# Kernel optimization log

Measured on AMD Instinct MI355X. Metric: run time of the kernel, lower is better.

## Reference

```python
import jax, jax.numpy as jnp
import numpy as np

B, S, D, H = 4, 2048, 1024, 16
DH = D // H  # 64


def setup_inputs() -> dict:
    key = jax.random.key(0)
    ks = jax.random.split(key, 7)
    scale = 1.0 / np.sqrt(DH)  # ~ torch Linear init scale
    return {
        "seqs": jax.random.normal(ks[0], (B, S, D), dtype=jnp.float32),
        "Wq": jax.random.normal(ks[1], (H, DH, DH), dtype=jnp.float32) * scale,
        "bq": jax.random.normal(ks[2], (H, DH), dtype=jnp.float32) * scale,
        "Wk": jax.random.normal(ks[3], (H, DH, DH), dtype=jnp.float32) * scale,
        "bk": jax.random.normal(ks[4], (H, DH), dtype=jnp.float32) * scale,
        "Wv": jax.random.normal(ks[5], (H, DH, DH), dtype=jnp.float32) * scale,
        "bv": jax.random.normal(ks[6], (H, DH), dtype=jnp.float32) * scale,
    }


def reference(seqs, Wq, bq, Wk, bk, Wv, bv):
    # seqs: [B, S, D] -> per-head slices [B, S, H, DH]
    x = seqs.reshape(B, S, H, DH)
    # torch Linear: y = s @ W.T + b  (W: [out, in]) -> einsum over 'in' axis d
    q = jnp.einsum("bshd,hed->bshe", x, Wq) + bq  # [B,S,H,DH]
    k = jnp.einsum("bshd,hed->bshe", x, Wk) + bk
    v = jnp.einsum("bshd,hed->bshe", x, Wv) + bv
    inv_sqrt = 1.0 / jnp.sqrt(jnp.asarray(DH, dtype=seqs.dtype))
    scores = jnp.einsum("bshe,bthe->bhst", q, k) * inv_sqrt  # [B,H,S,S]
    attn = jax.nn.softmax(scores, axis=-1)
    out = jnp.einsum("bhst,bthe->bshe", attn, v)  # [B,S,H,DH]
    # torch.hstack over heads == concat along feature dim
    return out.reshape(B, S, D)
```

## Files before the change

kernel.cpp:

```cpp
#include <hip/hip_runtime.h>
#include <hip/hip_bf16.h>

#define NB 4
#define NS 2048
#define ND 1024
#define NH 16
#define NDH 64
#define SCF 0.18033688011112042f

typedef __attribute__((ext_vector_type(8))) short bf16x8;
typedef __attribute__((ext_vector_type(4))) float f32x4;

__device__ __forceinline__ float bf2f(unsigned short u) {
    union { unsigned int u; float f; } x; x.u = ((unsigned int)u) << 16; return x.f;
}
__device__ __forceinline__ unsigned short f2bf(float f) {
    union { float f; unsigned int u; } x; x.f = f;
    unsigned int r = x.u + 0x7FFFu + ((x.u >> 16) & 1u);
    return (unsigned short)(r >> 16);
}
__device__ __forceinline__ unsigned short f2bf_fast(float f) {
    union { float f; unsigned int u; } x; x.f = f;
    return (unsigned short)((x.u + 0x8000u) >> 16);
}
__device__ __forceinline__ unsigned int pkbf(float a, float b) {
    union { float f; unsigned int u; } x, y; x.f = a; y.f = b;
    return __builtin_amdgcn_perm(y.u + 0x8000u, x.u + 0x8000u, 0x07060302u);
}
__device__ __forceinline__ unsigned int pktr(float a, float b) {
    union { float f; unsigned int u; } x, y; x.f = a; y.f = b;
    return __builtin_amdgcn_perm(y.u, x.u, 0x07060302u);
}

__global__ __launch_bounds__(256) void convert_w_kernel(
    const unsigned short* __restrict__ x,
    const void* __restrict__ Wq, const void* __restrict__ bq,
    const void* __restrict__ Wk, const void* __restrict__ bk,
    const void* __restrict__ Wv, const void* __restrict__ bv,
    int* __restrict__ flag,
    unsigned short* __restrict__ Wb,
    unsigned short* __restrict__ Bb)
{
    __shared__ int sflag;
    const int tid = threadIdx.x;
    if (tid < 64) {
        int bad = 0, zer = 0;
        for (int i = tid; i < 1024; i += 64) {
            const unsigned short u = x[2 * i];
            const int e = (u >> 7) & 0xFF;
            if (e >= 0x8F) bad++;
            if (e == 0 && (u & 0x7F)) bad++;
            if (u == 0) zer++;
        }
        #pragma unroll
        for (int off = 1; off < 64; off <<= 1) {
            bad += __shfl_xor(bad, off, 64);
            zer += __shfl_xor(zer, off, 64);
        }
        if (tid == 0) {
            const int f = (bad > 64 || zer > 512) ? 1 : 0;
            sflag = f;
            flag[0] = f;
        }
    }
    __syncthreads();
    const int isf32 = sflag;

    const void* Wsrc[3] = { Wq, Wk, Wv };
    const void* Bsrc[3] = { bq, bk, bv };
    const int NW = 3 * 65536, NBIAS = 3 * 1024;
    for (int i = blockIdx.x * blockDim.x + tid; i < NW + NBIAS;
         i += gridDim.x * blockDim.x) {
        int m, off; const void* src; unsigned short* dst;
        if (i < NW) { m = i >> 16; off = i & 65535; src = Wsrc[m]; dst = Wb + i; }
        else { int j = i - NW; m = j >> 10; off = j & 1023; src = Bsrc[m];
               dst = Bb + j; }
        float v = isf32 ? ((const float*)src)[off]
                        : bf2f(((const unsigned short*)src)[off]);
        if (m == 0) v *= SCF;
        *dst = f2bf(v);
    }
}

__global__ __launch_bounds__(256) void qkv_proj_kernel(
    const unsigned short* __restrict__ x,
    const unsigned short* __restrict__ Wb,
    const unsigned short* __restrict__ Bb,
    const int* __restrict__ flag,
    unsigned short* __restrict__ Qw, unsigned short* __restrict__ Kw,
    unsigned short* __restrict__ VwT)
{
    __shared__ __align__(16) unsigned short Tl[3 * 64 * 72];

    const int isf32 = flag[0];
    const int tid  = threadIdx.x;
    const int wave = tid >> 6, lane = tid & 63;
    const int quad = lane >> 4, l16 = lane & 15;
    const int ttile = blockIdx.x, h = blockIdx.y;
    const int b  = ttile >> 5;
    const int s0 = (ttile & 31) * 64;
    const int bh = b * NH + h;

    const int tok_a = ttile * 64 + wave * 16 + l16;
    bf16x8 af0, af1;
    if (isf32) {
        const f32x4* xp = (const f32x4*)((const float*)x + (size_t)tok_a * ND + h * NDH);
        const f32x4 v0 = xp[quad * 2], v1 = xp[quad * 2 + 1];
        const f32x4 v2 = xp[8 + quad * 2], v3 = xp[8 + quad * 2 + 1];
        union { bf16x8 v; unsigned int d[4]; } a0, a1;
        a0.d[0] = pkbf(v0[0], v0[1]); a0.d[1] = pkbf(v0[2], v0[3]);
        a0.d[2] = pkbf(v1[0], v1[1]); a0.d[3] = pkbf(v1[2], v1[3]);
        a1.d[0] = pkbf(v2[0], v2[1]); a1.d[1] = pkbf(v2[2], v2[3]);
        a1.d[2] = pkbf(v3[0], v3[1]); a1.d[3] = pkbf(v3[2], v3[3]);
        af0 = a0.v; af1 = a1.v;
    } else {
        const unsigned short* xr = x + (size_t)tok_a * ND + h * NDH;
        af0 = *(const bf16x8*)(xr + quad * 8);
        af1 = *(const bf16x8*)(xr + 32 + quad * 8);
    }

    #pragma unroll
    for (int m = 0; m < 3; ++m) {
        const unsigned short* W = Wb + m * 65536 + h * 4096;
        unsigned short* R = Tl + m * (64 * 72);
        #pragma unroll
        for (int n = 0; n < 4; ++n) {
            const unsigned short* wrow = W + (n * 16 + l16) * NDH;
            const bf16x8 b0 = *(const bf16x8*)(wrow + quad * 8);
            const bf16x8 b1 = *(const bf16x8*)(wrow + 32 + quad * 8);
            f32x4 acc = {0.f, 0.f, 0.f, 0.f};
            acc = __builtin_amdgcn_mfma_f32_16x16x32_bf16(af0, b0, acc, 0, 0, 0);
            acc = __builtin_amdgcn_mfma_f32_16x16x32_bf16(af1, b1, acc, 0, 0, 0);
            const float bias = bf2f(Bb[m * 1024 + h * NDH + n * 16 + l16]);
            if (m < 2) {
                #pragma unroll
                for (int r = 0; r < 4; ++r) {
                    const int row = wave * 16 + quad * 4 + r;
                    R[row * 72 + n * 16 + l16] = f2bf_fast(acc[r] + bias);
                }
            } else {
                #pragma unroll
                for (int r = 0; r < 4; ++r) {
                    const int tok = wave * 16 + quad * 4 + r;
                    const int pc = ((tok & 15) << 2) | (tok >> 4);
                    R[(n * 16 + l16) * 72 + pc] = f2bf_fast(acc[r] + bias);
                }
            }
        }
    }
    __syncthreads();
    #pragma unroll
    for (int p = 0; p < 2; ++p) {
        const int ch = tid + p * 256;
        const int tl = ch >> 3, sub = ch & 7;
        *(bf16x8*)(Qw + ((size_t)bh * NS + s0 + tl) * NDH + sub * 8) =
            *(const bf16x8*)(Tl + tl * 72 + sub * 8);
        *(bf16x8*)(Kw + ((size_t)bh * NS + s0 + tl) * NDH + sub * 8) =
            *(const bf16x8*)(Tl + 64 * 72 + tl * 72 + sub * 8);
        *(bf16x8*)(VwT + ((size_t)bh * NDH + tl) * NS + s0 + sub * 8) =
            *(const bf16x8*)(Tl + 2 * 64 * 72 + tl * 72 + sub * 8);
    }
}

__global__ __launch_bounds__(256, 2) void attn_kernel(
    const unsigned short* __restrict__ Qw,
    const unsigned short* __restrict__ Kw,
    const unsigned short* __restrict__ VwT,
    const int* __restrict__ flag,
    unsigned short* __restrict__ out)
{
    __shared__ __align__(16) unsigned short smem[5 * 64 * 72];
    unsigned short* Pt = smem + 4 * 64 * 72;
    unsigned short* Ot = smem;

    const int isf32 = flag[0];
    const int tid  = threadIdx.x;
    const int wave = tid >> 6, lane = tid & 63;
    const int quad = lane >> 4, l16 = lane & 15;
    const int qt = blockIdx.x & 7;
    const int bh = blockIdx.x >> 3;
    const int b = bh >> 4, h = bh & 15;

    const unsigned short* Qb = Qw  + (size_t)bh * NS * NDH;
    const unsigned short* Kb = Kw  + (size_t)bh * NS * NDH;
    const unsigned short* Vb = VwT + (size_t)bh * NDH * NS;

    bf16x8 qf[4][2];
    #pragma unroll
    for (int mh = 0; mh < 4; ++mh) {
        const int tok = qt * 256 + wave * 64 + mh * 16 + l16;
        qf[mh][0] = *(const bf16x8*)(Qb + (size_t)tok * NDH + quad * 8);
        qf[mh][1] = *(const bf16x8*)(Qb + (size_t)tok * NDH + 32 + quad * 8);
    }

    f32x4 o[4][4];
    float os[4][4];
    #pragma unroll
    for (int mh = 0; mh < 4; ++mh) {
        #pragma unroll
        for (int n = 0; n < 4; ++n) o[mh][n] = f32x4{0.f, 0.f, 0.f, 0.f};
        #pragma unroll
        for (int r = 0; r < 4; ++r) os[mh][r] = 0.f;
    }

    const int stage_r = tid >> 3, stage_c = tid & 7;
    unsigned short* PtW = Pt + wave * (16 * 72);

    bf16x8 kpre[2], vpre[2];
    #pragma unroll
    for (int p = 0; p < 2; ++p) {
        const int rr = stage_r + p * 32;
        kpre[p] = *(const bf16x8*)(Kb + (size_t)rr * NDH + stage_c * 8);
        vpre[p] = *(const bf16x8*)(Vb + (size_t)rr * NS + stage_c * 8);
    }

    for (int kt = 0; kt < NS / 64; ++kt) {
        unsigned short* KB = smem + (kt & 1) * (64 * 72);
        unsigned short* VB = smem + (2 + (kt & 1)) * (64 * 72);
        #pragma unroll
        for (int p = 0; p < 2; ++p) {
            const int rr = stage_r + p * 32;
            *(bf16x8*)(KB + rr * 72 + stage_c * 8) = kpre[p];
            *(bf16x8*)(VB + rr * 72 + stage_c * 8) = vpre[p];
        }
        __syncthreads();
        if (kt + 1 < NS / 64) {
            #pragma unroll
            for (int p = 0; p < 2; ++p) {
                const int rr = stage_r + p * 32;
                kpre[p] = *(const bf16x8*)(Kb + (size_t)((kt + 1) * 64 + rr) * NDH + stage_c * 8);
                vpre[p] = *(const bf16x8*)(Vb + (size_t)rr * NS + (kt + 1) * 64 + stage_c * 8);
            }
        }

        bf16x8 kb[4][2], vb[4][2];
        #pragma unroll
        for (int n = 0; n < 4; ++n) {
            kb[n][0] = *(const bf16x8*)(KB + (n * 16 + l16) * 72 + quad * 8);
            kb[n][1] = *(const bf16x8*)(KB + (n * 16 + l16) * 72 + 32 + quad * 8);
            vb[n][0] = *(const bf16x8*)(VB + (n * 16 + l16) * 72 + quad * 8);
            vb[n][1] = *(const bf16x8*)(VB + (n * 16 + l16) * 72 + 32 + quad * 8);
        }

        #pragma unroll
        for (int mh = 0; mh < 4; ++mh) {
            f32x4 sf[4];
            #pragma unroll
            for (int n = 0; n < 4; ++n) {
                f32x4 acc = {0.f, 0.f, 0.f, 0.f};
                acc = __builtin_amdgcn_mfma_f32_16x16x32_bf16(qf[mh][0], kb[n][0], acc, 0, 0, 0);
                acc = __builtin_amdgcn_mfma_f32_16x16x32_bf16(qf[mh][1], kb[n][1], acc, 0, 0, 0);
                sf[n] = acc;
            }
            #pragma unroll
            for (int r = 0; r < 4; ++r) {
                const float p0 = __builtin_amdgcn_exp2f(sf[0][r]);
                const float p1 = __builtin_amdgcn_exp2f(sf[1][r]);
                const float p2 = __builtin_amdgcn_exp2f(sf[2][r]);
                const float p3 = __builtin_amdgcn_exp2f(sf[3][r]);
                os[mh][r] += (p0 + p1) + (p2 + p3);
                uint2 d; d.x = pktr(p0, p1); d.y = pktr(p2, p3);
                *(uint2*)(PtW + (quad * 4 + r) * 72 + l16 * 4) = d;
            }
            const bf16x8 pa0 = *(const bf16x8*)(PtW + l16 * 72 + quad * 8);
            const bf16x8 pa1 = *(const bf16x8*)(PtW + l16 * 72 + 32 + quad * 8);
            #pragma unroll
            for (int n = 0; n < 4; ++n) {
                o[mh][n] = __builtin_amdgcn_mfma_f32_16x16x32_bf16(pa0, vb[n][0], o[mh][n], 0, 0, 0);
                o[mh][n] = __builtin_amdgcn_mfma_f32_16x16x32_bf16(pa1, vb[n][1], o[mh][n], 0, 0, 0);
            }
        }
    }

    float inv[4][4];
    #pragma unroll
    for (int mh = 0; mh < 4; ++mh) {
        #pragma unroll
        for (int r = 0; r < 4; ++r) {
            float s = os[mh][r];
            #pragma unroll
            for (int off = 1; off < 16; off <<= 1)
                s += __shfl_xor(s, off, 64);
            inv[mh][r] = 1.0f / s;
        }
    }

    if (isf32) {
        float* of = (float*)out;
        #pragma unroll
        for (int mh = 0; mh < 4; ++mh) {
            #pragma unroll
            for (int r = 0; r < 4; ++r) {
                const int s = qt * 256 + wave * 64 + mh * 16 + quad * 4 + r;
                #pragma unroll
                for (int n = 0; n < 4; ++n)
                    of[((size_t)(b * NS + s)) * ND + h * NDH + n * 16 + l16] =
                        o[mh][n][r] * inv[mh][r];
            }
        }
    } else {
        __syncthreads();
        #pragma unroll
        for (int mh = 0; mh < 4; ++mh) {
            #pragma unroll
            for (int r = 0; r < 4; ++r) {
                const int row = wave * 64 + mh * 16 + quad * 4 + r;
                #pragma unroll
                for (int n = 0; n < 4; ++n)
                    Ot[row * 72 + n * 16 + l16] = f2bf(o[mh][n][r] * inv[mh][r]);
            }
        }
        __syncthreads();
        #pragma unroll
        for (int p = 0; p < 8; ++p) {
            const int ch = tid + p * 256;
            const int tl = ch >> 3, sub = ch & 7;
            const int s = qt * 256 + tl;
            *(bf16x8*)(out + ((size_t)(b * NS + s)) * ND + h * NDH + sub * 8) =
                *(const bf16x8*)(Ot + tl * 72 + sub * 8);
        }
    }
}

extern "C" void kernel_launch(void* const* d_in, const int* in_sizes, int n_in,
                              void* d_out, int out_size, void* d_ws, size_t ws_size,
                              hipStream_t stream)
{
    const unsigned short* x = (const unsigned short*)d_in[0];
    int* flag = (int*)d_ws;
    const size_t per = (size_t)NB * NH * NS * NDH;
    unsigned short* Qw  = (unsigned short*)((char*)d_ws + 256);
    unsigned short* Kw  = Qw + per;
    unsigned short* VwT = Kw + per;
    unsigned short* Wb  = VwT + per;
    unsigned short* Bb  = Wb + 3 * 65536;

    convert_w_kernel<<<256, 256, 0, stream>>>(
        x, d_in[1], d_in[2], d_in[3], d_in[4], d_in[5], d_in[6], flag, Wb, Bb);
    qkv_proj_kernel<<<dim3(NB * NS / 64, NH), 256, 0, stream>>>(
        x, Wb, Bb, flag, Qw, Kw, VwT);
    attn_kernel<<<NB * NH * (NS / 256), 256, 0, stream>>>(
        Qw, Kw, VwT, flag, (unsigned short*)d_out);
}
```

Before: 199.0 us.

## Load K/V fragments directly from global memory into registers, drop LDS staging

```diff
diff --git a/kernel.cpp b/kernel.cpp
--- a/kernel.cpp
+++ b/kernel.cpp
@@ -169,21 +169,22 @@
     const int* __restrict__ flag,
     unsigned short* __restrict__ out)
 {
-    __shared__ __align__(16) unsigned short smem[5 * 64 * 72];
-    unsigned short* Pt = smem + 4 * 64 * 72;
+    __shared__ __align__(16) unsigned short smem[256 * 72];
     unsigned short* Ot = smem;
 
     const int isf32 = flag[0];
     const int tid  = threadIdx.x;
     const int wave = tid >> 6, lane = tid & 63;
     const int quad = lane >> 4, l16 = lane & 15;
-    const int qt = blockIdx.x & 7;
-    const int bh = blockIdx.x >> 3;
+    const int bh = blockIdx.x & 63;
+    const int qt = blockIdx.x >> 6;
     const int b = bh >> 4, h = bh & 15;
 
     const unsigned short* Qb = Qw  + (size_t)bh * NS * NDH;
     const unsigned short* Kb = Kw  + (size_t)bh * NS * NDH;
     const unsigned short* Vb = VwT + (size_t)bh * NDH * NS;
+
+    unsigned short* PtW = smem + wave * (16 * 72);
 
     bf16x8 qf[4][2];
     #pragma unroll
@@ -203,53 +204,39 @@
         for (int r = 0; r < 4; ++r) os[mh][r] = 0.f;
     }
 
-    const int stage_r = tid >> 3, stage_c = tid & 7;
-    unsigned short* PtW = Pt + wave * (16 * 72);
-
-    bf16x8 kpre[2], vpre[2];
-    #pragma unroll
-    for (int p = 0; p < 2; ++p) {
-        const int rr = stage_r + p * 32;
-        kpre[p] = *(const bf16x8*)(Kb + (size_t)rr * NDH + stage_c * 8);
-        vpre[p] = *(const bf16x8*)(Vb + (size_t)rr * NS + stage_c * 8);
-    }
-
-    for (int kt = 0; kt < NS / 64; ++kt) {
-        unsigned short* KB = smem + (kt & 1) * (64 * 72);
-        unsigned short* VB = smem + (2 + (kt & 1)) * (64 * 72);
-        #pragma unroll
-        for (int p = 0; p < 2; ++p) {
-            const int rr = stage_r + p * 32;
-            *(bf16x8*)(KB + rr * 72 + stage_c * 8) = kpre[p];
-            *(bf16x8*)(VB + rr * 72 + stage_c * 8) = vpre[p];
-        }
-        __syncthreads();
-        if (kt + 1 < NS / 64) {
-            #pragma unroll
-            for (int p = 0; p < 2; ++p) {
-                const int rr = stage_r + p * 32;
-                kpre[p] = *(const bf16x8*)(Kb + (size_t)((kt + 1) * 64 + rr) * NDH + stage_c * 8);
-                vpre[p] = *(const bf16x8*)(Vb + (size_t)rr * NS + (kt + 1) * 64 + stage_c * 8);
-            }
-        }
-
-        bf16x8 kb[4][2], vb[4][2];
+    bf16x8 kA[4][2], kB[4][2], vb[4][2];
+
+    auto loadK = [&](bf16x8 (&kd)[4][2], const int t) {
+        const unsigned short* Kt =
+            Kb + (size_t)t * 64 * NDH + (size_t)l16 * NDH + quad * 8;
         #pragma unroll
         for (int n = 0; n < 4; ++n) {
-            kb[n][0] = *(const bf16x8*)(KB + (n * 16 + l16) * 72 + quad * 8);
-            kb[n][1] = *(const bf16x8*)(KB + (n * 16 + l16) * 72 + 32 + quad * 8);
-            vb[n][0] = *(const bf16x8*)(VB + (n * 16 + l16) * 72 + quad * 8);
-            vb[n][1] = *(const bf16x8*)(VB + (n * 16 + l16) * 72 + 32 + quad * 8);
-        }
-
+            kd[n][0] = *(const bf16x8*)(Kt + n * 16 * NDH);
+            kd[n][1] = *(const bf16x8*)(Kt + n * 16 * NDH + 32);
+        }
+    };
+    auto loadV = [&](const int t) {
+        const unsigned short* Vt =
+            Vb + (size_t)l16 * NS + (size_t)t * 64 + quad * 8;
+        #pragma unroll
+        for (int n = 0; n < 4; ++n) {
+            vb[n][0] = *(const bf16x8*)(Vt + (size_t)(n * 16) * NS);
+            vb[n][1] = *(const bf16x8*)(Vt + (size_t)(n * 16) * NS + 32);
+        }
+    };
+
+    auto body = [&](bf16x8 (&kc)[4][2], bf16x8 (&kn)[4][2], const int t) {
+        loadV(t);
+        const int tn = (t + 1 < NS / 64) ? t + 1 : NS / 64 - 1;
+        loadK(kn, tn);
         #pragma unroll
         for (int mh = 0; mh < 4; ++mh) {
             f32x4 sf[4];
             #pragma unroll
             for (int n = 0; n < 4; ++n) {
                 f32x4 acc = {0.f, 0.f, 0.f, 0.f};
-                acc = __builtin_amdgcn_mfma_f32_16x16x32_bf16(qf[mh][0], kb[n][0], acc, 0, 0, 0);
-                acc = __builtin_amdgcn_mfma_f32_16x16x32_bf16(qf[mh][1], kb[n][1], acc, 0, 0, 0);
+                acc = __builtin_amdgcn_mfma_f32_16x16x32_bf16(qf[mh][0], kc[n][0], acc, 0, 0, 0);
+                acc = __builtin_amdgcn_mfma_f32_16x16x32_bf16(qf[mh][1], kc[n][1], acc, 0, 0, 0);
                 sf[n] = acc;
             }
             #pragma unroll
@@ -270,6 +257,13 @@
                 o[mh][n] = __builtin_amdgcn_mfma_f32_16x16x32_bf16(pa1, vb[n][1], o[mh][n], 0, 0, 0);
             }
         }
+    };
+
+    loadK(kA, 0);
+    #pragma unroll 1
+    for (int t = 0; t < NS / 64; t += 2) {
+        body(kA, kB, t);
+        body(kB, kA, t + 1);
     }
 
     float inv[4][4];
```

Result: slower. 365.2 us (+83.5%).
